# Kernel tuning notes

Hardware: AMD Instinct MI355X
Metric: run time of the kernel (lower is better)

The kernel has to match this reference:

```python
import jax, jax.numpy as jnp
import numpy as np

L, B, T, D, H, DH, DFF, S = 4, 64, 511, 1024, 16, 64, 4096, 256
SCALE = 1.0 / np.sqrt(DH)
EPS = 1e-5


def _ln(x, g, b):
    m = x.mean(-1, keepdims=True)
    v = ((x - m) ** 2).mean(-1, keepdims=True)
    return (x - m) * jax.lax.rsqrt(v + EPS) * g + b


def setup_inputs() -> dict:
    key = jax.random.key(0)
    ks = jax.random.split(key, 24)
    wp = 0.02  # weight init scale to keep activations sane
    r = lambda k, shp, s: jax.random.normal(k, shp, jnp.float32) * s
    return {
        'tgt_last': r(ks[0], (1, B, D), 1.0),
        'cache': r(ks[1], (L, T, B, D), 1.0),
        'K0': r(ks[2], (B, H, T, DH), 1.0),
        'V0': r(ks[3], (B, H, T, DH), 1.0),
        'K_mem': r(ks[4], (L, B, H, S, DH), 1.0),
        'V_mem': r(ks[5], (L, B, H, S, DH), 1.0),
        'sa_W': r(ks[6], (L, 3 * D, D), wp), 'sa_b': r(ks[7], (L, 3 * D), wp),
        'sa_oW': r(ks[8], (L, D, D), wp), 'sa_ob': r(ks[9], (L, D), wp),
        'ca_qW': r(ks[10], (L, D, D), wp), 'ca_qb': r(ks[11], (L, D), wp),
        'ca_oW': r(ks[12], (L, D, D), wp), 'ca_ob': r(ks[13], (L, D), wp),
        'W1': r(ks[14], (L, DFF, D), wp), 'b1': r(ks[15], (L, DFF), wp),
        'W2': r(ks[16], (L, D, DFF), wp), 'b2': r(ks[17], (L, D), wp),
        'ln1_g': jnp.ones((L, D), jnp.float32), 'ln1_b': jnp.zeros((L, D), jnp.float32),
        'ln2_g': jnp.ones((L, D), jnp.float32), 'ln2_b': jnp.zeros((L, D), jnp.float32),
        'ln3_g': jnp.ones((L, D), jnp.float32), 'ln3_b': jnp.zeros((L, D), jnp.float32),
    }


def reference(tgt_last, cache, K0, V0, K_mem, V_mem, sa_W, sa_b, sa_oW, sa_ob,
              ca_qW, ca_qb, ca_oW, ca_ob, W1, b1, W2, b2,
              ln1_g, ln1_b, ln2_g, ln2_b, ln3_g, ln3_b):
    # One incremental decode step through L decoder layers (eval mode, dropout=0).
    x = tgt_last  # [1,B,D]
    for i in range(L):
        last = x
        Wq, Wk, Wv = sa_W[i, :D], sa_W[i, D:2 * D], sa_W[i, 2 * D:]
        bq, bk, bv = sa_b[i, :D], sa_b[i, D:2 * D], sa_b[i, 2 * D:]
        q = (last[0] @ Wq.T + bq).reshape(B, H, DH)  # [B,H,Dh]
        if i == 0:
            # _sa_kv_step: project only the new token, append to cached K/V
            k = (last[0] @ Wk.T + bk).reshape(B, H, 1, DH)
            v = (last[0] @ Wv.T + bv).reshape(B, H, 1, DH)
            K = jnp.concatenate([K0, k], axis=2)  # [B,H,T+1,Dh]
            V = jnp.concatenate([V0, v], axis=2)
        else:
            # standard self-attn: K/V from full prefix concat(cache[i], x)
            tgt_i = jnp.concatenate([cache[i], x], axis=0)  # [T+1,B,D]
            K = (tgt_i @ Wk.T + bk).reshape(T + 1, B, H, DH).transpose(1, 2, 0, 3)
            V = (tgt_i @ Wv.T + bv).reshape(T + 1, B, H, DH).transpose(1, 2, 0, 3)
        s = jnp.einsum('bhd,bhtd->bht', q, K) * SCALE
        a = jax.nn.softmax(s, axis=-1)
        ctx = jnp.einsum('bht,bhtd->bhd', a, V).reshape(B, D)[None]  # [1,B,D]
        sa = ctx @ sa_oW[i].T + sa_ob[i]
        x = _ln(last + sa, ln1_g[i], ln1_b[i])
        # cross-attention against precomputed memory K/V
        qc = (x[0] @ ca_qW[i].T + ca_qb[i]).reshape(B, H, DH)
        sc = jnp.einsum('bhd,bhsd->bhs', qc, K_mem[i]) * SCALE
        ac = jax.nn.softmax(sc, axis=-1)
        cc = jnp.einsum('bhs,bhsd->bhd', ac, V_mem[i]).reshape(B, D)[None]
        cc = cc @ ca_oW[i].T + ca_ob[i]
        x = _ln(x + cc, ln2_g[i], ln2_b[i])
        # FFN (relu, the nn.TransformerDecoderLayer default)
        ff = jax.nn.relu(x @ W1[i].T + b1[i]) @ W2[i].T + b2[i]
        x = _ln(x + ff, ln3_g[i], ln3_b[i])
    return x  # [1,B,D] embedding of the newly decoded token
```

## Files before the change

### kernel.cpp

```cpp
#include <hip/hip_runtime.h>
#include <math.h>

#define B 64
#define D 1024
#define H 16
#define DH 64
#define T 511
#define TT 512
#define SMEM 256
#define DFF 4096
#define NLAYER 4
#define SCALE 0.125f
#define EPS 1e-5f

__device__ __forceinline__ float dot4(const float4 a, const float4 b) {
    return a.x * b.x + a.y * b.y + a.z * b.z + a.w * b.w;
}
__device__ __forceinline__ float4 f4add(float4 a, float4 b) {
    return make_float4(a.x + b.x, a.y + b.y, a.z + b.z, a.w + b.w);
}

template <int K, int KS>
__global__ __launch_bounds__(256) void gemm_proj(
    const float* __restrict__ A,
    const float* __restrict__ W,
    float* __restrict__ P)
{
    constexpr int KSUB = K / KS;
    const int O = gridDim.x * 128;
    const int obase = blockIdx.x * 128;
    const int kb = blockIdx.y * KSUB;
    const int tid = threadIdx.x;

    __shared__ float As[32][68];
    __shared__ float Ws[32][132];

    const int b0 = (tid >> 4) * 4;
    const int o0 = (tid & 15) * 8;

    float acc[4][8];
#pragma unroll
    for (int i = 0; i < 4; ++i)
#pragma unroll
        for (int j = 0; j < 8; ++j) acc[i][j] = 0.f;

    for (int kc = 0; kc < KSUB; kc += 32) {
#pragma unroll
        for (int j = 0; j < 2; ++j) {
            const int f = tid + 256 * j;
            const int bb = f >> 3, k4 = f & 7;
            const float4 v = *reinterpret_cast<const float4*>(
                A + (size_t)bb * K + kb + kc + 4 * k4);
            As[4 * k4 + 0][bb] = v.x; As[4 * k4 + 1][bb] = v.y;
            As[4 * k4 + 2][bb] = v.z; As[4 * k4 + 3][bb] = v.w;
        }
#pragma unroll
        for (int j = 0; j < 4; ++j) {
            const int f = tid + 256 * j;
            const int oo = f >> 3, k4 = f & 7;
            const float4 v = *reinterpret_cast<const float4*>(
                W + (size_t)(obase + oo) * K + kb + kc + 4 * k4);
            Ws[4 * k4 + 0][oo] = v.x; Ws[4 * k4 + 1][oo] = v.y;
            Ws[4 * k4 + 2][oo] = v.z; Ws[4 * k4 + 3][oo] = v.w;
        }
        __syncthreads();
#pragma unroll 8
        for (int k = 0; k < 32; ++k) {
            const float4 av = *reinterpret_cast<const float4*>(&As[k][b0]);
            const float4 w0 = *reinterpret_cast<const float4*>(&Ws[k][o0]);
            const float4 w1 = *reinterpret_cast<const float4*>(&Ws[k][o0 + 4]);
            const float a[4] = {av.x, av.y, av.z, av.w};
            const float w[8] = {w0.x, w0.y, w0.z, w0.w, w1.x, w1.y, w1.z, w1.w};
#pragma unroll
            for (int i = 0; i < 4; ++i)
#pragma unroll
                for (int j = 0; j < 8; ++j)
                    acc[i][j] = fmaf(a[i], w[j], acc[i][j]);
        }
        __syncthreads();
    }

    float* Pb = P + (size_t)blockIdx.y * 64 * O;
#pragma unroll
    for (int i = 0; i < 4; ++i) {
        const float4 v0 = make_float4(acc[i][0], acc[i][1], acc[i][2], acc[i][3]);
        const float4 v1 = make_float4(acc[i][4], acc[i][5], acc[i][6], acc[i][7]);
        *reinterpret_cast<float4*>(Pb + (size_t)(b0 + i) * O + obase + o0) = v0;
        *reinterpret_cast<float4*>(Pb + (size_t)(b0 + i) * O + obase + o0 + 4) = v1;
    }
}

__global__ __launch_bounds__(256) void gemm_ffn2(
    const float* __restrict__ Pffn,
    const float* __restrict__ b1v,
    const float* __restrict__ W,
    float* __restrict__ P)
{
    constexpr int K = DFF, KS = 32, KSUB = K / KS;
    const int obase = blockIdx.x * 128;
    const int kb = blockIdx.y * KSUB;
    const int tid = threadIdx.x;

    __shared__ float As[32][68];
    __shared__ float Ws[32][132];

    const int b0 = (tid >> 4) * 4;
    const int o0 = (tid & 15) * 8;

    float acc[4][8];
#pragma unroll
    for (int i = 0; i < 4; ++i)
#pragma unroll
        for (int j = 0; j < 8; ++j) acc[i][j] = 0.f;

    for (int kc = 0; kc < KSUB; kc += 32) {
#pragma unroll
        for (int j = 0; j < 2; ++j) {
            const int f = tid + 256 * j;
            const int bb = f >> 3, k4 = f & 7;
            const int kg = kb + kc + 4 * k4;
            float4 v = *reinterpret_cast<const float4*>(b1v + kg);
#pragma unroll
            for (int s = 0; s < 8; ++s)
                v = f4add(v, *reinterpret_cast<const float4*>(
                    Pffn + (size_t)(s * 64 + bb) * K + kg));
            v.x = fmaxf(v.x, 0.f); v.y = fmaxf(v.y, 0.f);
            v.z = fmaxf(v.z, 0.f); v.w = fmaxf(v.w, 0.f);
            As[4 * k4 + 0][bb] = v.x; As[4 * k4 + 1][bb] = v.y;
            As[4 * k4 + 2][bb] = v.z; As[4 * k4 + 3][bb] = v.w;
        }
#pragma unroll
        for (int j = 0; j < 4; ++j) {
            const int f = tid + 256 * j;
            const int oo = f >> 3, k4 = f & 7;
            const float4 v = *reinterpret_cast<const float4*>(
                W + (size_t)(obase + oo) * K + kb + kc + 4 * k4);
            Ws[4 * k4 + 0][oo] = v.x; Ws[4 * k4 + 1][oo] = v.y;
            Ws[4 * k4 + 2][oo] = v.z; Ws[4 * k4 + 3][oo] = v.w;
        }
        __syncthreads();
#pragma unroll 8
        for (int k = 0; k < 32; ++k) {
            const float4 av = *reinterpret_cast<const float4*>(&As[k][b0]);
            const float4 w0 = *reinterpret_cast<const float4*>(&Ws[k][o0]);
            const float4 w1 = *reinterpret_cast<const float4*>(&Ws[k][o0 + 4]);
            const float a[4] = {av.x, av.y, av.z, av.w};
            const float w[8] = {w0.x, w0.y, w0.z, w0.w, w1.x, w1.y, w1.z, w1.w};
#pragma unroll
            for (int i = 0; i < 4; ++i)
#pragma unroll
                for (int j = 0; j < 8; ++j)
                    acc[i][j] = fmaf(a[i], w[j], acc[i][j]);
        }
        __syncthreads();
    }

    float* Pb = P + (size_t)blockIdx.y * 64 * D;
#pragma unroll
    for (int i = 0; i < 4; ++i) {
        const float4 v0 = make_float4(acc[i][0], acc[i][1], acc[i][2], acc[i][3]);
        const float4 v1 = make_float4(acc[i][4], acc[i][5], acc[i][6], acc[i][7]);
        *reinterpret_cast<float4*>(Pb + (size_t)(b0 + i) * D + obase + o0) = v0;
        *reinterpret_cast<float4*>(Pb + (size_t)(b0 + i) * D + obase + o0 + 4) = v1;
    }
}

__global__ __launch_bounds__(256) void gemm_u(
    const float* __restrict__ Pq,
    const float* __restrict__ bq,
    const float* __restrict__ Wk,
    float* __restrict__ u)
{
    const int h = blockIdx.x;
    const int dbase = blockIdx.y * 128;
    const int tid = threadIdx.x;

    __shared__ float As[32][68];
    __shared__ float Ws[32][132];

    const int b0 = (tid >> 4) * 4;
    const int o0 = (tid & 15) * 8;

    float acc[4][8];
#pragma unroll
    for (int i = 0; i < 4; ++i)
#pragma unroll
        for (int j = 0; j < 8; ++j) acc[i][j] = 0.f;

    for (int kc = 0; kc < DH; kc += 32) {
#pragma unroll
        for (int j = 0; j < 2; ++j) {
            const int f = tid + 256 * j;
            const int bb = f >> 3, k4 = f & 7;
            const int kg = h * DH + kc + 4 * k4;
            float4 v = *reinterpret_cast<const float4*>(bq + kg);
#pragma unroll
            for (int s = 0; s < 16; ++s)
                v = f4add(v, *reinterpret_cast<const float4*>(
                    Pq + (size_t)(s * 64 + bb) * D + kg));
            As[4 * k4 + 0][bb] = v.x; As[4 * k4 + 1][bb] = v.y;
            As[4 * k4 + 2][bb] = v.z; As[4 * k4 + 3][bb] = v.w;
        }
#pragma unroll
        for (int j = 0; j < 4; ++j) {
            const int f = tid + 256 * j;
            const int k = f >> 5, d4 = f & 31;
            const float4 v = *reinterpret_cast<const float4*>(
                Wk + (size_t)(h * DH + kc + k) * D + dbase + 4 * d4);
            *reinterpret_cast<float4*>(&Ws[k][4 * d4]) = v;
        }
        __syncthreads();
#pragma unroll 8
        for (int k = 0; k < 32; ++k) {
            const float4 av = *reinterpret_cast<const float4*>(&As[k][b0]);
            const float4 w0 = *reinterpret_cast<const float4*>(&Ws[k][o0]);
            const float4 w1 = *reinterpret_cast<const float4*>(&Ws[k][o0 + 4]);
            const float a[4] = {av.x, av.y, av.z, av.w};
            const float w[8] = {w0.x, w0.y, w0.z, w0.w, w1.x, w1.y, w1.z, w1.w};
#pragma unroll
            for (int i = 0; i < 4; ++i)
#pragma unroll
                for (int j = 0; j < 8; ++j)
                    acc[i][j] = fmaf(a[i], w[j], acc[i][j]);
        }
        __syncthreads();
    }
#pragma unroll
    for (int i = 0; i < 4; ++i) {
        const float4 v0 = make_float4(acc[i][0], acc[i][1], acc[i][2], acc[i][3]);
        const float4 v1 = make_float4(acc[i][4], acc[i][5], acc[i][6], acc[i][7]);
        float* ur = u + ((size_t)(b0 + i) * H + h) * D + dbase + o0;
        *reinterpret_cast<float4*>(ur) = v0;
        *reinterpret_cast<float4*>(ur + 4) = v1;
    }
}

__global__ __launch_bounds__(512) void sattn_kernel(
    const float* __restrict__ cache_i, const float* __restrict__ x,
    const float* __restrict__ u, float* __restrict__ wpart4,
    float* __restrict__ sums)
{
    const int b = blockIdx.x, th = blockIdx.y;
    const int tid = threadIdx.x;
    const int h = tid >> 5, seg = tid & 31;

    float4 ur[8];
    const float* ub = u + ((size_t)(b * H + h)) * D;
#pragma unroll
    for (int c = 0; c < 8; ++c) {
        const float4 v = *reinterpret_cast<const float4*>(ub + c * 128 + seg * 4);
        ur[c] = make_float4(v.x * SCALE, v.y * SCALE, v.z * SCALE, v.w * SCALE);
    }
    float4 ar[8];
#pragma unroll
    for (int c = 0; c < 8; ++c) ar[c] = make_float4(0.f, 0.f, 0.f, 0.f);
    float sumE = 0.f;

    __shared__ float rowb[2][1024];

    const int tg0 = th * 128;
    float2 pre;
    {
        const float* row = (tg0 < T) ? cache_i + ((size_t)tg0 * B + b) * D
                                     : x + (size_t)b * D;
        pre = *reinterpret_cast<const float2*>(row + tid * 2);
    }

    for (int tt = 0; tt < 128; ++tt) {
        const int cur = tt & 1;
        *reinterpret_cast<float2*>(&rowb[cur][tid * 2]) = pre;
        __syncthreads();
        if (tt + 1 < 128) {
            const int t = tg0 + tt + 1;
            const float* row = (t < T) ? cache_i + ((size_t)t * B + b) * D
                                       : x + (size_t)b * D;
            pre = *reinterpret_cast<const float2*>(row + tid * 2);
        }
        float4 rv[8];
        float dot = 0.f;
#pragma unroll
        for (int c = 0; c < 8; ++c) {
            rv[c] = *reinterpret_cast<const float4*>(&rowb[cur][c * 128 + seg * 4]);
            dot += dot4(ur[c], rv[c]);
        }
#pragma unroll
        for (int m = 16; m >= 1; m >>= 1) dot += __shfl_xor(dot, m, 64);
        const float e = __expf(dot);
        sumE += e;
#pragma unroll
        for (int c = 0; c < 8; ++c) {
            ar[c].x = fmaf(e, rv[c].x, ar[c].x);
            ar[c].y = fmaf(e, rv[c].y, ar[c].y);
            ar[c].z = fmaf(e, rv[c].z, ar[c].z);
            ar[c].w = fmaf(e, rv[c].w, ar[c].w);
        }
    }

    float* wp = wpart4 + (((size_t)(b * 4 + th)) * H + h) * D;
#pragma unroll
    for (int c = 0; c < 8; ++c)
        *reinterpret_cast<float4*>(wp + c * 128 + seg * 4) = ar[c];
    if (seg == 0) sums[(b * 4 + th) * H + h] = sumE;
}

__global__ __launch_bounds__(256) void gemm_ctx4(
    const float* __restrict__ wpart4, const float* __restrict__ sums,
    const float* __restrict__ Wv, float* __restrict__ P)
{
    constexpr int KSUB = D / 4;
    const int h = blockIdx.x;
    const int kb = blockIdx.y * KSUB;
    const int tid = threadIdx.x;

    __shared__ float As[32][68];
    __shared__ float Ws[32][68];
    __shared__ float sinv[64];

    if (tid < 64) {
        float s = 0.f;
#pragma unroll
        for (int t = 0; t < 4; ++t) s += sums[(tid * 4 + t) * H + h];
        sinv[tid] = 1.f / s;
    }
    __syncthreads();

    const int b0 = (tid >> 4) * 4;
    const int o0 = (tid & 15) * 4;

    float acc[4][4];
#pragma unroll
    for (int i = 0; i < 4; ++i)
#pragma unroll
        for (int j = 0; j < 4; ++j) acc[i][j] = 0.f;

    for (int kc = 0; kc < KSUB; kc += 32) {
#pragma unroll
        for (int j = 0; j < 2; ++j) {
            const int f = tid + 256 * j;
            const int bb = f >> 3, k4 = f & 7;
            float4 v = make_float4(0.f, 0.f, 0.f, 0.f);
#pragma unroll
            for (int t = 0; t < 4; ++t)
                v = f4add(v, *reinterpret_cast<const float4*>(
                    wpart4 + (((size_t)(bb * 4 + t)) * H + h) * D + kb + kc + 4 * k4));
            const float iv = sinv[bb];
            As[4 * k4 + 0][bb] = v.x * iv; As[4 * k4 + 1][bb] = v.y * iv;
            As[4 * k4 + 2][bb] = v.z * iv; As[4 * k4 + 3][bb] = v.w * iv;
        }
#pragma unroll
        for (int j = 0; j < 2; ++j) {
            const int f = tid + 256 * j;
            const int oo = f >> 3, k4 = f & 7;
            const float4 v = *reinterpret_cast<const float4*>(
                Wv + (size_t)(h * DH + oo) * D + kb + kc + 4 * k4);
            Ws[4 * k4 + 0][oo] = v.x; Ws[4 * k4 + 1][oo] = v.y;
            Ws[4 * k4 + 2][oo] = v.z; Ws[4 * k4 + 3][oo] = v.w;
        }
        __syncthreads();
#pragma unroll 8
        for (int k = 0; k < 32; ++k) {
            const float4 av = *reinterpret_cast<const float4*>(&As[k][b0]);
            const float4 wv = *reinterpret_cast<const float4*>(&Ws[k][o0]);
            const float a[4] = {av.x, av.y, av.z, av.w};
            const float w[4] = {wv.x, wv.y, wv.z, wv.w};
#pragma unroll
            for (int i = 0; i < 4; ++i)
#pragma unroll
                for (int j = 0; j < 4; ++j)
                    acc[i][j] = fmaf(a[i], w[j], acc[i][j]);
        }
        __syncthreads();
    }
    float* Pb = P + (size_t)blockIdx.y * 64 * D;
#pragma unroll
    for (int i = 0; i < 4; ++i) {
        const float4 v = make_float4(acc[i][0], acc[i][1], acc[i][2], acc[i][3]);
        *reinterpret_cast<float4*>(Pb + (size_t)(b0 + i) * D + h * DH + o0) = v;
    }
}

template <int KS, bool RELU, int O>
__global__ __launch_bounds__(256) void finish_plain(
    const float* __restrict__ P, const float* __restrict__ bias,
    float* __restrict__ out)
{
    constexpr int OC = O / 4;
    const int e = blockIdx.x * 256 + threadIdx.x;
    const int oc = e % OC;
    const int b = e / OC;
    const float4* P4 = reinterpret_cast<const float4*>(P);
    float4 a = reinterpret_cast<const float4*>(bias)[oc];
#pragma unroll
    for (int s = 0; s < KS; ++s)
        a = f4add(a, P4[(size_t)(s * 64 + b) * OC + oc]);
    if (RELU) {
        a.x = fmaxf(a.x, 0.f); a.y = fmaxf(a.y, 0.f);
        a.z = fmaxf(a.z, 0.f); a.w = fmaxf(a.w, 0.f);
    }
    reinterpret_cast<float4*>(out)[e] = a;
}

template <int KS>
__global__ __launch_bounds__(256) void finish_ln(
    const float* __restrict__ P, const float* __restrict__ bias,
    const float* __restrict__ resid, const float* __restrict__ g,
    const float* __restrict__ bb, float* __restrict__ out)
{
    const int b = blockIdx.x, tid = threadIdx.x;
    const float4* P4 = reinterpret_cast<const float4*>(P);
    float4 v = reinterpret_cast<const float4*>(bias)[tid];
    v = f4add(v, reinterpret_cast<const float4*>(resid + (size_t)b * D)[tid]);
#pragma unroll
    for (int s = 0; s < KS; ++s)
        v = f4add(v, P4[(size_t)(s * 64 + b) * 256 + tid]);

    float ssum = v.x + v.y + v.z + v.w;
#pragma unroll
    for (int m = 32; m >= 1; m >>= 1) ssum += __shfl_xor(ssum, m, 64);
    __shared__ float red[4];
    if ((tid & 63) == 0) red[tid >> 6] = ssum;
    __syncthreads();
    const float mean = (red[0] + red[1] + red[2] + red[3]) * (1.f / D);
    const float dx = v.x - mean, dy = v.y - mean, dz = v.z - mean, dw = v.w - mean;
    float q = dx * dx + dy * dy + dz * dz + dw * dw;
#pragma unroll
    for (int m = 32; m >= 1; m >>= 1) q += __shfl_xor(q, m, 64);
    __shared__ float red2[4];
    if ((tid & 63) == 0) red2[tid >> 6] = q;
    __syncthreads();
    const float var = (red2[0] + red2[1] + red2[2] + red2[3]) * (1.f / D);
    const float rs = rsqrtf(var + EPS);
    const float4 gv = reinterpret_cast<const float4*>(g)[tid];
    const float4 bv = reinterpret_cast<const float4*>(bb)[tid];
    float4 o;
    o.x = dx * rs * gv.x + bv.x;
    o.y = dy * rs * gv.y + bv.y;
    o.z = dz * rs * gv.z + bv.z;
    o.w = dw * rs * gv.w + bv.w;
    reinterpret_cast<float4*>(out + (size_t)b * D)[tid] = o;
}

template <int NS>
__global__ __launch_bounds__(256) void attn_kernel(
    const float* __restrict__ q, const float* __restrict__ Kb,
    const float* __restrict__ Vb, const float* __restrict__ extraK,
    const float* __restrict__ extraV, float* __restrict__ ctx,
    int nk, int qpitch)
{
    const int b = blockIdx.x, h = blockIdx.y, tid = threadIdx.x;
    __shared__ float qs[DH];
    __shared__ float sa[NS];
    if (tid < DH) qs[tid] = q[(size_t)b * qpitch + h * DH + tid];
    __syncthreads();

    const int ss = tid >> 2, p = tid & 3;
    const float* Kbh = Kb + ((size_t)(b * H + h)) * nk * DH;
#pragma unroll 2
    for (int pass = 0; pass < NS / 64; ++pass) {
        const int s = pass * 64 + ss;
        const float* row = (s < nk) ? (Kbh + (size_t)s * DH)
                                    : (extraK + (size_t)b * qpitch + h * DH);
        const float4* rp = reinterpret_cast<const float4*>(row);
        const float4* qp = reinterpret_cast<const float4*>(qs) + p * 4;
        float acc = 0.f;
#pragma unroll
        for (int c = 0; c < 4; ++c) acc += dot4(rp[p * 4 + c], qp[c]);
        acc += __shfl_xor(acc, 1, 64);
        acc += __shfl_xor(acc, 2, 64);
        if (p == 0) sa[s] = acc * SCALE;
    }
    __syncthreads();

    float m = -1e30f;
    for (int k = tid; k < NS; k += 256) m = fmaxf(m, sa[k]);
#pragma unroll
    for (int mm = 32; mm >= 1; mm >>= 1) m = fmaxf(m, __shfl_xor(m, mm, 64));
    __shared__ float r1[4];
    if ((tid & 63) == 0) r1[tid >> 6] = m;
    __syncthreads();
    m = fmaxf(fmaxf(r1[0], r1[1]), fmaxf(r1[2], r1[3]));
    float sum = 0.f;
    for (int k = tid; k < NS; k += 256) {
        const float e = __expf(sa[k] - m);
        sa[k] = e;
        sum += e;
    }
#pragma unroll
    for (int mm = 32; mm >= 1; mm >>= 1) sum += __shfl_xor(sum, mm, 64);
    __shared__ float r2[4];
    if ((tid & 63) == 0) r2[tid >> 6] = sum;
    __syncthreads();
    const float inv = 1.f / (r2[0] + r2[1] + r2[2] + r2[3]);

    const int dh4 = tid & 15, sq = tid >> 4;
    const float* Vbh = Vb + ((size_t)(b * H + h)) * nk * DH;
    float4 acc = make_float4(0.f, 0.f, 0.f, 0.f);
#pragma unroll 2
    for (int s = sq; s < NS; s += 16) {
        const float* row = (s < nk) ? (Vbh + (size_t)s * DH)
                                    : (extraV + (size_t)b * qpitch + h * DH);
        const float4 vv = *reinterpret_cast<const float4*>(row + dh4 * 4);
        const float av = sa[s];
        acc.x += av * vv.x; acc.y += av * vv.y;
        acc.z += av * vv.z; acc.w += av * vv.w;
    }
    __shared__ float red[16 * 68];
    *reinterpret_cast<float4*>(&red[sq * 68 + dh4 * 4]) = acc;
    __syncthreads();
    if (tid < 64) {
        float t = 0.f;
#pragma unroll
        for (int k = 0; k < 16; ++k) t += red[k * 68 + tid];
        ctx[(size_t)b * D + h * DH + tid] = t * inv;
    }
}

extern "C" void kernel_launch(void* const* d_in, const int* in_sizes, int n_in,
                              void* d_out, int out_size, void* d_ws, size_t ws_size,
                              hipStream_t stream)
{
    const float* tgt_last = (const float*)d_in[0];
    const float* cache    = (const float*)d_in[1];
    const float* K0       = (const float*)d_in[2];
    const float* V0       = (const float*)d_in[3];
    const float* K_mem    = (const float*)d_in[4];
    const float* V_mem    = (const float*)d_in[5];
    const float* sa_W     = (const float*)d_in[6];
    const float* sa_b     = (const float*)d_in[7];
    const float* sa_oW    = (const float*)d_in[8];
    const float* sa_ob    = (const float*)d_in[9];
    const float* ca_qW    = (const float*)d_in[10];
    const float* ca_qb    = (const float*)d_in[11];
    const float* ca_oW    = (const float*)d_in[12];
    const float* ca_ob    = (const float*)d_in[13];
    const float* W1       = (const float*)d_in[14];
    const float* b1       = (const float*)d_in[15];
    const float* W2       = (const float*)d_in[16];
    const float* b2       = (const float*)d_in[17];
    const float* ln1_g    = (const float*)d_in[18];
    const float* ln1_b    = (const float*)d_in[19];
    const float* ln2_g    = (const float*)d_in[20];
    const float* ln2_b    = (const float*)d_in[21];
    const float* ln3_g    = (const float*)d_in[22];
    const float* ln3_b    = (const float*)d_in[23];

    float* ws = (float*)d_ws;
    float* x_buf   = ws;
    float* q_buf   = ws + 65536;
    float* ctx_buf = ws + 131072;
    float* qkv_buf = ws + 196608;
    float* u_buf   = ws + 393216;
    float* wpart4  = ws + 1441792;
    float* sums    = ws + 5636096;
    float* Pq      = ws + 5640192;
    float* Pqkv    = ws + 6688768;
    float* Pc      = ws + 8261632;
    float* Pffn    = ws + 8523776;
    float* Pffn2   = ws + 10620928;

    const dim3 blk(256);

    for (int i = 0; i < NLAYER; ++i) {
        const float* x = (i == 0) ? tgt_last : x_buf;
        const float* Wq = sa_W + (size_t)i * 3 * D * D;
        const float* Wk = Wq + (size_t)D * D;
        const float* Wv = Wq + (size_t)2 * D * D;
        const float* bq = sa_b + (size_t)i * 3 * D;
        const float* bv = bq + 2 * D;

        if (i == 0) {
            gemm_proj<D, 8><<<dim3(24, 8), blk, 0, stream>>>(x, Wq, Pqkv);
            finish_plain<8, false, 3072><<<dim3(192), blk, 0, stream>>>(
                Pqkv, bq, qkv_buf);
            attn_kernel<TT><<<dim3(B, H), blk, 0, stream>>>(
                qkv_buf, K0, V0, qkv_buf + 1024, qkv_buf + 2048, ctx_buf, T, 3072);
        } else {
            const float* cache_i = cache + (size_t)i * T * B * D;
            gemm_proj<D, 16><<<dim3(8, 16), blk, 0, stream>>>(x, Wq, Pq);
            gemm_u<<<dim3(H, 8), blk, 0, stream>>>(Pq, bq, Wk, u_buf);
            sattn_kernel<<<dim3(B, 4), dim3(512), 0, stream>>>(
                cache_i, x, u_buf, wpart4, sums);
            gemm_ctx4<<<dim3(H, 4), blk, 0, stream>>>(wpart4, sums, Wv, Pc);
            finish_plain<4, false, D><<<dim3(64), blk, 0, stream>>>(
                Pc, bv, ctx_buf);
        }

        gemm_proj<D, 16><<<dim3(8, 16), blk, 0, stream>>>(
            ctx_buf, sa_oW + (size_t)i * D * D, Pq);
        finish_ln<16><<<dim3(B), blk, 0, stream>>>(
            Pq, sa_ob + (size_t)i * D, x, ln1_g + (size_t)i * D,
            ln1_b + (size_t)i * D, x_buf);

        gemm_proj<D, 16><<<dim3(8, 16), blk, 0, stream>>>(
            x_buf, ca_qW + (size_t)i * D * D, Pq);
        finish_plain<16, false, D><<<dim3(64), blk, 0, stream>>>(
            Pq, ca_qb + (size_t)i * D, q_buf);
        attn_kernel<SMEM><<<dim3(B, H), blk, 0, stream>>>(
            q_buf, K_mem + (size_t)i * B * H * SMEM * DH,
            V_mem + (size_t)i * B * H * SMEM * DH,
            q_buf, q_buf, ctx_buf, SMEM, 1024);
        gemm_proj<D, 16><<<dim3(8, 16), blk, 0, stream>>>(
            ctx_buf, ca_oW + (size_t)i * D * D, Pq);
        finish_ln<16><<<dim3(B), blk, 0, stream>>>(
            Pq, ca_ob + (size_t)i * D, x_buf, ln2_g + (size_t)i * D,
            ln2_b + (size_t)i * D, x_buf);

        gemm_proj<D, 8><<<dim3(32, 8), blk, 0, stream>>>(
            x_buf, W1 + (size_t)i * DFF * D, Pffn);
        gemm_ffn2<<<dim3(8, 32), blk, 0, stream>>>(
            Pffn, b1 + (size_t)i * DFF, W2 + (size_t)i * D * DFF, Pffn2);
        float* lnout = (i == NLAYER - 1) ? (float*)d_out : x_buf;
        finish_ln<32><<<dim3(B), blk, 0, stream>>>(
            Pffn2, b2 + (size_t)i * D, x_buf, ln3_g + (size_t)i * D,
            ln3_b + (size_t)i * D, lnout);
    }
}
```

Measured before the change: 931.8 us.

## Fuse partial-sum reductions into consumer kernels and deepen split-K for small GEMMs

Removes the finish_plain reduction kernels by folding the split-K partial sums and bias into the consumers: the attention kernel reads q/k/v partials directly, and a generic gemm_psum sums ctx partials on load for the out-projection. Split-K for the D×D projections goes from 16 to 32 and the value GEMM from 4 to 8 splits, giving more blocks. The self-attention streaming kernel now stages two cache rows per barrier with float4 loads, halving syncs. This cuts launches and round-trips through global memory, at the cost of more partial-sum traffic and redundant reduction work inside consumers.

```diff
diff --git a/kernel.cpp b/kernel.cpp
--- a/kernel.cpp
+++ b/kernel.cpp
@@ -90,13 +90,15 @@
     }
 }
 
-__global__ __launch_bounds__(256) void gemm_ffn2(
-    const float* __restrict__ Pffn,
-    const float* __restrict__ b1v,
+template <int K, int KS, int NPART, bool RELU_A>
+__global__ __launch_bounds__(256) void gemm_psum(
+    const float* __restrict__ Pa,
+    const float* __restrict__ abias,
     const float* __restrict__ W,
     float* __restrict__ P)
 {
-    constexpr int K = DFF, KS = 32, KSUB = K / KS;
+    constexpr int KSUB = K / KS;
+    const int O = gridDim.x * 128;
     const int obase = blockIdx.x * 128;
     const int kb = blockIdx.y * KSUB;
     const int tid = threadIdx.x;
@@ -119,13 +121,15 @@
             const int f = tid + 256 * j;
             const int bb = f >> 3, k4 = f & 7;
             const int kg = kb + kc + 4 * k4;
-            float4 v = *reinterpret_cast<const float4*>(b1v + kg);
-#pragma unroll
-            for (int s = 0; s < 8; ++s)
+            float4 v = *reinterpret_cast<const float4*>(abias + kg);
+#pragma unroll
+            for (int s = 0; s < NPART; ++s)
                 v = f4add(v, *reinterpret_cast<const float4*>(
-                    Pffn + (size_t)(s * 64 + bb) * K + kg));
-            v.x = fmaxf(v.x, 0.f); v.y = fmaxf(v.y, 0.f);
-            v.z = fmaxf(v.z, 0.f); v.w = fmaxf(v.w, 0.f);
+                    Pa + (size_t)(s * 64 + bb) * K + kg));
+            if (RELU_A) {
+                v.x = fmaxf(v.x, 0.f); v.y = fmaxf(v.y, 0.f);
+                v.z = fmaxf(v.z, 0.f); v.w = fmaxf(v.w, 0.f);
+            }
             As[4 * k4 + 0][bb] = v.x; As[4 * k4 + 1][bb] = v.y;
             As[4 * k4 + 2][bb] = v.z; As[4 * k4 + 3][bb] = v.w;
         }
@@ -155,13 +159,13 @@
         __syncthreads();
     }
 
-    float* Pb = P + (size_t)blockIdx.y * 64 * D;
+    float* Pb = P + (size_t)blockIdx.y * 64 * O;
 #pragma unroll
     for (int i = 0; i < 4; ++i) {
         const float4 v0 = make_float4(acc[i][0], acc[i][1], acc[i][2], acc[i][3]);
         const float4 v1 = make_float4(acc[i][4], acc[i][5], acc[i][6], acc[i][7]);
-        *reinterpret_cast<float4*>(Pb + (size_t)(b0 + i) * D + obase + o0) = v0;
-        *reinterpret_cast<float4*>(Pb + (size_t)(b0 + i) * D + obase + o0 + 4) = v1;
+        *reinterpret_cast<float4*>(Pb + (size_t)(b0 + i) * O + obase + o0) = v0;
+        *reinterpret_cast<float4*>(Pb + (size_t)(b0 + i) * O + obase + o0 + 4) = v1;
     }
 }
 
@@ -256,43 +260,45 @@
     for (int c = 0; c < 8; ++c) ar[c] = make_float4(0.f, 0.f, 0.f, 0.f);
     float sumE = 0.f;
 
-    __shared__ float rowb[2][1024];
+    __shared__ float rowb[2][2][1024];
 
     const int tg0 = th * 128;
-    float2 pre;
-    {
-        const float* row = (tg0 < T) ? cache_i + ((size_t)tg0 * B + b) * D
-                                     : x + (size_t)b * D;
-        pre = *reinterpret_cast<const float2*>(row + tid * 2);
-    }
-
-    for (int tt = 0; tt < 128; ++tt) {
-        const int cur = tt & 1;
-        *reinterpret_cast<float2*>(&rowb[cur][tid * 2]) = pre;
-        __syncthreads();
-        if (tt + 1 < 128) {
-            const int t = tg0 + tt + 1;
-            const float* row = (t < T) ? cache_i + ((size_t)t * B + b) * D
-                                       : x + (size_t)b * D;
-            pre = *reinterpret_cast<const float2*>(row + tid * 2);
-        }
-        float4 rv[8];
-        float dot = 0.f;
-#pragma unroll
-        for (int c = 0; c < 8; ++c) {
-            rv[c] = *reinterpret_cast<const float4*>(&rowb[cur][c * 128 + seg * 4]);
-            dot += dot4(ur[c], rv[c]);
-        }
-#pragma unroll
-        for (int m = 16; m >= 1; m >>= 1) dot += __shfl_xor(dot, m, 64);
-        const float e = __expf(dot);
-        sumE += e;
-#pragma unroll
-        for (int c = 0; c < 8; ++c) {
-            ar[c].x = fmaf(e, rv[c].x, ar[c].x);
-            ar[c].y = fmaf(e, rv[c].y, ar[c].y);
-            ar[c].z = fmaf(e, rv[c].z, ar[c].z);
-            ar[c].w = fmaf(e, rv[c].w, ar[c].w);
+    const int lr = tid >> 8;
+    const int lc = (tid & 255) * 4;
+
+    auto rowptr = [&](int t) -> const float* {
+        return (t < T) ? cache_i + ((size_t)t * B + b) * D : x + (size_t)b * D;
+    };
+    float4 pre = *reinterpret_cast<const float4*>(rowptr(tg0 + lr) + lc);
+
+    for (int st = 0; st < 64; ++st) {
+        const int p = st & 1;
+        *reinterpret_cast<float4*>(&rowb[p][lr][lc]) = pre;
+        __syncthreads();
+        if (st + 1 < 64)
+            pre = *reinterpret_cast<const float4*>(
+                rowptr(tg0 + 2 * (st + 1) + lr) + lc);
+#pragma unroll
+        for (int r = 0; r < 2; ++r) {
+            float4 rv[8];
+            float dot = 0.f;
+#pragma unroll
+            for (int c = 0; c < 8; ++c) {
+                rv[c] = *reinterpret_cast<const float4*>(
+                    &rowb[p][r][c * 128 + seg * 4]);
+                dot += dot4(ur[c], rv[c]);
+            }
+#pragma unroll
+            for (int m = 16; m >= 1; m >>= 1) dot += __shfl_xor(dot, m, 64);
+            const float e = __expf(dot);
+            sumE += e;
+#pragma unroll
+            for (int c = 0; c < 8; ++c) {
+                ar[c].x = fmaf(e, rv[c].x, ar[c].x);
+                ar[c].y = fmaf(e, rv[c].y, ar[c].y);
+                ar[c].z = fmaf(e, rv[c].z, ar[c].z);
+                ar[c].w = fmaf(e, rv[c].w, ar[c].w);
+            }
         }
     }
 
@@ -303,11 +309,11 @@
     if (seg == 0) sums[(b * 4 + th) * H + h] = sumE;
 }
 
-__global__ __launch_bounds__(256) void gemm_ctx4(
+__global__ __launch_bounds__(256) void gemm_ctx8(
     const float* __restrict__ wpart4, const float* __restrict__ sums,
     const float* __restrict__ Wv, float* __restrict__ P)
 {
-    constexpr int KSUB = D / 4;
+    constexpr int KSUB = D / 8;
     const int h = blockIdx.x;
     const int kb = blockIdx.y * KSUB;
     const int tid = threadIdx.x;
@@ -338,11 +344,12 @@
         for (int j = 0; j < 2; ++j) {
             const int f = tid + 256 * j;
             const int bb = f >> 3, k4 = f & 7;
+            const int kg = kb + kc + 4 * k4;
             float4 v = make_float4(0.f, 0.f, 0.f, 0.f);
 #pragma unroll
             for (int t = 0; t < 4; ++t)
                 v = f4add(v, *reinterpret_cast<const float4*>(
-                    wpart4 + (((size_t)(bb * 4 + t)) * H + h) * D + kb + kc + 4 * k4));
+                    wpart4 + (((size_t)(bb * 4 + t)) * H + h) * D + kg));
             const float iv = sinv[bb];
             As[4 * k4 + 0][bb] = v.x * iv; As[4 * k4 + 1][bb] = v.y * iv;
             As[4 * k4 + 2][bb] = v.z * iv; As[4 * k4 + 3][bb] = v.w * iv;
@@ -377,27 +384,6 @@
         const float4 v = make_float4(acc[i][0], acc[i][1], acc[i][2], acc[i][3]);
         *reinterpret_cast<float4*>(Pb + (size_t)(b0 + i) * D + h * DH + o0) = v;
     }
-}
-
-template <int KS, bool RELU, int O>
-__global__ __launch_bounds__(256) void finish_plain(
-    const float* __restrict__ P, const float* __restrict__ bias,
-    float* __restrict__ out)
-{
-    constexpr int OC = O / 4;
-    const int e = blockIdx.x * 256 + threadIdx.x;
-    const int oc = e % OC;
-    const int b = e / OC;
-    const float4* P4 = reinterpret_cast<const float4*>(P);
-    float4 a = reinterpret_cast<const float4*>(bias)[oc];
-#pragma unroll
-    for (int s = 0; s < KS; ++s)
-        a = f4add(a, P4[(size_t)(s * 64 + b) * OC + oc]);
-    if (RELU) {
-        a.x = fmaxf(a.x, 0.f); a.y = fmaxf(a.y, 0.f);
-        a.z = fmaxf(a.z, 0.f); a.w = fmaxf(a.w, 0.f);
-    }
-    reinterpret_cast<float4*>(out)[e] = a;
 }
 
 template <int KS>
@@ -440,17 +426,35 @@
     reinterpret_cast<float4*>(out + (size_t)b * D)[tid] = o;
 }
 
-template <int NS>
+template <int NS, bool HASX>
 __global__ __launch_bounds__(256) void attn_kernel(
-    const float* __restrict__ q, const float* __restrict__ Kb,
-    const float* __restrict__ Vb, const float* __restrict__ extraK,
-    const float* __restrict__ extraV, float* __restrict__ ctx,
-    int nk, int qpitch)
+    const float* __restrict__ qP, const float* __restrict__ qbias,
+    int qnp, int qpitch,
+    const float* __restrict__ Kb, const float* __restrict__ Vb,
+    float* __restrict__ ctx, int nk)
 {
     const int b = blockIdx.x, h = blockIdx.y, tid = threadIdx.x;
     __shared__ float qs[DH];
+    __shared__ float kx[DH];
+    __shared__ float vx[DH];
     __shared__ float sa[NS];
-    if (tid < DH) qs[tid] = q[(size_t)b * qpitch + h * DH + tid];
+    if (tid < DH) {
+        const int col = h * DH + tid;
+        float v = qbias[col];
+        for (int s = 0; s < qnp; ++s)
+            v += qP[(size_t)(s * 64 + b) * qpitch + col];
+        qs[tid] = v;
+        if (HASX) {
+            float kk = qbias[D + col];
+            float vv = qbias[2 * D + col];
+            for (int s = 0; s < qnp; ++s) {
+                const float* base = qP + (size_t)(s * 64 + b) * qpitch + col;
+                kk += base[D];
+                vv += base[2 * D];
+            }
+            kx[tid] = kk; vx[tid] = vv;
+        }
+    }
     __syncthreads();
 
     const int ss = tid >> 2, p = tid & 3;
@@ -458,8 +462,8 @@
 #pragma unroll 2
     for (int pass = 0; pass < NS / 64; ++pass) {
         const int s = pass * 64 + ss;
-        const float* row = (s < nk) ? (Kbh + (size_t)s * DH)
-                                    : (extraK + (size_t)b * qpitch + h * DH);
+        const float* row = (!HASX || s < nk) ? (Kbh + (size_t)s * DH)
+                                             : (const float*)kx;
         const float4* rp = reinterpret_cast<const float4*>(row);
         const float4* qp = reinterpret_cast<const float4*>(qs) + p * 4;
         float acc = 0.f;
@@ -497,8 +501,8 @@
     float4 acc = make_float4(0.f, 0.f, 0.f, 0.f);
 #pragma unroll 2
     for (int s = sq; s < NS; s += 16) {
-        const float* row = (s < nk) ? (Vbh + (size_t)s * DH)
-                                    : (extraV + (size_t)b * qpitch + h * DH);
+        const float* row = (!HASX || s < nk) ? (Vbh + (size_t)s * DH)
+                                             : (const float*)vx;
         const float4 vv = *reinterpret_cast<const float4*>(row + dh4 * 4);
         const float av = sa[s];
         acc.x += av * vv.x; acc.y += av * vv.y;
@@ -546,72 +550,67 @@
 
     float* ws = (float*)d_ws;
     float* x_buf   = ws;
-    float* q_buf   = ws + 65536;
-    float* ctx_buf = ws + 131072;
-    float* qkv_buf = ws + 196608;
-    float* u_buf   = ws + 393216;
-    float* wpart4  = ws + 1441792;
-    float* sums    = ws + 5636096;
-    float* Pq      = ws + 5640192;
-    float* Pqkv    = ws + 6688768;
-    float* Pc      = ws + 8261632;
-    float* Pffn    = ws + 8523776;
-    float* Pffn2   = ws + 10620928;
+    float* ctx_buf = ws + 65536;
+    float* u_buf   = ws + 131072;
+    float* wpart4  = ws + 1179648;
+    float* sums    = ws + 5373952;
+    float* Pq      = ws + 5378048;
+    float* PqA     = ws + 6426624;
+    float* Pqkv    = ws + 8523776;
+    float* Pc      = ws + 10096640;
+    float* Pffn    = ws + 10620928;
+    float* Pffn2   = ws + 12718080;
 
     const dim3 blk(256);
 
     for (int i = 0; i < NLAYER; ++i) {
-        const float* x = (i == 0) ? tgt_last : x_buf;
-        const float* Wq = sa_W + (size_t)i * 3 * D * D;
-        const float* Wk = Wq + (size_t)D * D;
-        const float* Wv = Wq + (size_t)2 * D * D;
-        const float* bq = sa_b + (size_t)i * 3 * D;
-        const float* bv = bq + 2 * D;
+        const float* Wq   = sa_W + (size_t)i * 3 * D * D;
+        const float* bqkv = sa_b + (size_t)i * 3 * D;
 
         if (i == 0) {
-            gemm_proj<D, 8><<<dim3(24, 8), blk, 0, stream>>>(x, Wq, Pqkv);
-            finish_plain<8, false, 3072><<<dim3(192), blk, 0, stream>>>(
-                Pqkv, bq, qkv_buf);
-            attn_kernel<TT><<<dim3(B, H), blk, 0, stream>>>(
-                qkv_buf, K0, V0, qkv_buf + 1024, qkv_buf + 2048, ctx_buf, T, 3072);
+            gemm_proj<D, 8><<<dim3(24, 8), blk, 0, stream>>>(tgt_last, Wq, Pqkv);
+            attn_kernel<TT, true><<<dim3(B, H), blk, 0, stream>>>(
+                Pqkv, bqkv, 8, 3 * D, K0, V0, ctx_buf, T);
+            gemm_proj<D, 32><<<dim3(8, 32), blk, 0, stream>>>(
+                ctx_buf, sa_oW + (size_t)i * D * D, PqA);
+            finish_ln<32><<<dim3(B), blk, 0, stream>>>(
+                PqA, sa_ob + (size_t)i * D, tgt_last,
+                ln1_g + (size_t)i * D, ln1_b + (size_t)i * D, x_buf);
         } else {
             const float* cache_i = cache + (size_t)i * T * B * D;
-            gemm_proj<D, 16><<<dim3(8, 16), blk, 0, stream>>>(x, Wq, Pq);
-            gemm_u<<<dim3(H, 8), blk, 0, stream>>>(Pq, bq, Wk, u_buf);
+            gemm_proj<D, 16><<<dim3(8, 16), blk, 0, stream>>>(x_buf, Wq, Pq);
+            gemm_u<<<dim3(H, 8), blk, 0, stream>>>(
+                Pq, bqkv, Wq + (size_t)D * D, u_buf);
             sattn_kernel<<<dim3(B, 4), dim3(512), 0, stream>>>(
-                cache_i, x, u_buf, wpart4, sums);
-            gemm_ctx4<<<dim3(H, 4), blk, 0, stream>>>(wpart4, sums, Wv, Pc);
-            finish_plain<4, false, D><<<dim3(64), blk, 0, stream>>>(
-                Pc, bv, ctx_buf);
-        }
-
-        gemm_proj<D, 16><<<dim3(8, 16), blk, 0, stream>>>(
-            ctx_buf, sa_oW + (size_t)i * D * D, Pq);
-        finish_ln<16><<<dim3(B), blk, 0, stream>>>(
-            Pq, sa_ob + (size_t)i * D, x, ln1_g + (size_t)i * D,
-            ln1_b + (size_t)i * D, x_buf);
-
-        gemm_proj<D, 16><<<dim3(8, 16), blk, 0, stream>>>(
-            x_buf, ca_qW + (size_t)i * D * D, Pq);
-        finish_plain<16, false, D><<<dim3(64), blk, 0, stream>>>(
-            Pq, ca_qb + (size_t)i * D, q_buf);
-        attn_kernel<SMEM><<<dim3(B, H), blk, 0, stream>>>(
-            q_buf, K_mem + (size_t)i * B * H * SMEM * DH,
-            V_mem + (size_t)i * B * H * SMEM * DH,
-            q_buf, q_buf, ctx_buf, SMEM, 1024);
-        gemm_proj<D, 16><<<dim3(8, 16), blk, 0, stream>>>(
-            ctx_buf, ca_oW + (size_t)i * D * D, Pq);
-        finish_ln<16><<<dim3(B), blk, 0, stream>>>(
-            Pq, ca_ob + (size_t)i * D, x_buf, ln2_g + (size_t)i * D,
-            ln2_b + (size_t)i * D, x_buf);
+                cache_i, x_buf, u_buf, wpart4, sums);
+            gemm_ctx8<<<dim3(H, 8), blk, 0, stream>>>(
+                wpart4, sums, Wq + (size_t)2 * D * D, Pc);
+            gemm_psum<D, 32, 8, false><<<dim3(8, 32), blk, 0, stream>>>(
+                Pc, bqkv + 2 * D, sa_oW + (size_t)i * D * D, PqA);
+            finish_ln<32><<<dim3(B), blk, 0, stream>>>(
+                PqA, sa_ob + (size_t)i * D, x_buf,
+                ln1_g + (size_t)i * D, ln1_b + (size_t)i * D, x_buf);
+        }
+
+        gemm_proj<D, 32><<<dim3(8, 32), blk, 0, stream>>>(
+            x_buf, ca_qW + (size_t)i * D * D, PqA);
+        attn_kernel<SMEM, false><<<dim3(B, H), blk, 0, stream>>>(
+            PqA, ca_qb + (size_t)i * D, 32, D,
+            K_mem + (size_t)i * B * H * SMEM * DH,
+            V_mem + (size_t)i * B * H * SMEM * DH, ctx_buf, SMEM);
+        gemm_proj<D, 32><<<dim3(8, 32), blk, 0, stream>>>(
+            ctx_buf, ca_oW + (size_t)i * D * D, PqA);
+        finish_ln<32><<<dim3(B), blk, 0, stream>>>(
+            PqA, ca_ob + (size_t)i * D, x_buf,
+            ln2_g + (size_t)i * D, ln2_b + (size_t)i * D, x_buf);
 
         gemm_proj<D, 8><<<dim3(32, 8), blk, 0, stream>>>(
             x_buf, W1 + (size_t)i * DFF * D, Pffn);
-        gemm_ffn2<<<dim3(8, 32), blk, 0, stream>>>(
+        gemm_psum<DFF, 32, 8, true><<<dim3(8, 32), blk, 0, stream>>>(
             Pffn, b1 + (size_t)i * DFF, W2 + (size_t)i * D * DFF, Pffn2);
         float* lnout = (i == NLAYER - 1) ? (float*)d_out : x_buf;
         finish_ln<32><<<dim3(B), blk, 0, stream>>>(
-            Pffn2, b2 + (size_t)i * D, x_buf, ln3_g + (size_t)i * D,
-            ln3_b + (size_t)i * D, lnout);
-    }
-}
+            Pffn2, b2 + (size_t)i * D, x_buf,
+            ln3_g + (size_t)i * D, ln3_b + (size_t)i * D, lnout);
+    }
+}
```

New measurement: 937.6 us. Within noise of the previous version (+0.6%).
